# Performance work log

Measured on AMD Instinct MI355X. Metric: run time of the kernel, lower is better.

The kernel has to match this reference:

```python
import jax, jax.numpy as jnp
import numpy as np

BETA = 0.9
THRESH = 1.0
SLOPE = 25.0  # fast_sigmoid surrogate slope

@jax.custom_vjp
def spike(x):
    # forward: heaviside(mem - threshold); backward: fast-sigmoid surrogate
    return (x > 0).astype(x.dtype)

def _spike_fwd(x):
    return (x > 0).astype(x.dtype), x

def _spike_bwd(x, g):
    return (g / (SLOPE * jnp.abs(x) + 1.0) ** 2,)

spike.defvjp(_spike_fwd, _spike_bwd)

def lif_step(mem, cur):
    # snntorch Leaky, reset_mechanism='subtract': reset from previous mem (detached)
    reset = jax.lax.stop_gradient((mem > THRESH).astype(cur.dtype))
    mem_new = BETA * mem + cur - reset * THRESH
    spk = spike(mem_new - THRESH)
    return spk, mem_new

def setup_inputs() -> dict:
    key = jax.random.key(0)
    ks = jax.random.split(key, 10)
    B, S, T = 256, 8, 25
    A, V, H, E = 512, 512, 256, 128
    a_seq = (jax.random.uniform(ks[0], (B, S, T, A)) < 0.2).astype(jnp.float32)
    v_seq = (jax.random.uniform(ks[1], (B, S, T, V)) < 0.2).astype(jnp.float32)
    def lin(kw, kb, out_d, in_d):
        lim = 1.0 / np.sqrt(in_d)
        W = jax.random.uniform(kw, (out_d, in_d), minval=-lim, maxval=lim, dtype=jnp.float32)
        b = jax.random.uniform(kb, (out_d,), minval=-lim, maxval=lim, dtype=jnp.float32)
        return W, b
    W_a1, b_a1 = lin(ks[2], ks[3], H, A)
    W_a2, b_a2 = lin(ks[4], ks[5], E, H)
    W_v1, b_v1 = lin(ks[6], ks[7], H, V)
    W_v2, b_v2 = lin(ks[8], ks[9], E, H)
    return dict(a_seq=a_seq, v_seq=v_seq, W_a1=W_a1, b_a1=b_a1, W_a2=W_a2, b_a2=b_a2,
                W_v1=W_v1, b_v1=b_v1, W_v2=W_v2, b_v2=b_v2)

def reference(a_seq, v_seq, W_a1, b_a1, W_a2, b_a2, W_v1, b_v1, W_v2, b_v2):
    B, S, T, A = a_seq.shape
    V = v_seq.shape[-1]
    H = W_a1.shape[0]
    E = W_a2.shape[0]
    BS = B * S  # segments are independent -> fold into batch
    a = a_seq.reshape(BS, T, A).transpose(1, 0, 2)  # [T, BS, A]
    v = v_seq.reshape(BS, T, V).transpose(1, 0, 2)  # [T, BS, V]

    def step(carry, xs):
        ma1, ma2, mv1, mv2, _, _ = carry
        at, vt = xs
        spk_a1, ma1 = lif_step(ma1, at @ W_a1.T + b_a1)
        spk_a2, ma2 = lif_step(ma2, spk_a1 @ W_a2.T + b_a2)
        spk_v1, mv1 = lif_step(mv1, vt @ W_v1.T + b_v1)
        spk_v2, mv2 = lif_step(mv2, spk_v1 @ W_v2.T + b_v2)
        return (ma1, ma2, mv1, mv2, spk_a2, spk_v2), None

    z = jnp.zeros
    init = (z((BS, H)), z((BS, E)), z((BS, H)), z((BS, E)), z((BS, E)), z((BS, E)))
    (ma1, ma2, mv1, mv2, spk_a2, spk_v2), _ = jax.lax.scan(step, init, (a, v))
    combined = jnp.concatenate([spk_a2, spk_v2], axis=1)  # [BS, 2E]
    norm = jnp.linalg.norm(combined, axis=1, keepdims=True)
    combined = combined / jnp.maximum(norm, 1e-12)  # F.normalize p=2 dim=1
    embs = combined.reshape(B, S, 2 * E)
    return embs.mean(axis=1)  # [B, 2E]
```

## Files before the change

### kernel.cpp

```cpp
#include <hip/hip_runtime.h>


typedef short bf16x8 __attribute__((ext_vector_type(8)));
typedef float f32x4 __attribute__((ext_vector_type(4)));

#define RBIG 51200

__global__ void prep_w(const float* __restrict__ Wa1, const float* __restrict__ Wv1,
                       const float* __restrict__ Wa2, const float* __restrict__ Wv2,
                       unsigned short* __restrict__ W1s, unsigned short* __restrict__ W2s) {
    int idx = blockIdx.x * 256 + threadIdx.x;
    float w;
    unsigned short* dst;
    int K, k;
    if (idx < 262144) {
        int p = idx >> 17, rem = idx & 131071;
        int n = rem >> 9; k = rem & 511; K = 512;
        const float* src = p ? Wv1 : Wa1;
        w = src[(size_t)n * 512 + k];
        dst = W1s + (size_t)p * 256 * 1536 + (size_t)n * 1536;
    } else {
        int j = idx - 262144;
        int p = j >> 15, rem = j & 32767;
        int n = rem >> 8; k = rem & 255; K = 256;
        const float* src = p ? Wv2 : Wa2;
        w = src[(size_t)n * 256 + k];
        dst = W2s + (size_t)p * 128 * 768 + (size_t)n * 768;
    }
    unsigned int u  = __float_as_uint(w);
    unsigned int hi = u & 0xFFFF0000u;
    float r1 = w - __uint_as_float(hi);
    unsigned int mi = __float_as_uint(r1) & 0xFFFF0000u;
    float r2 = r1 - __uint_as_float(mi);
    dst[k]         = (unsigned short)(hi >> 16);
    dst[K + k]     = (unsigned short)(mi >> 16);
    dst[2 * K + k] = (unsigned short)(__float_as_uint(r2) >> 16);
}

template <int KSRC, int NT, bool AF32>
__global__ __launch_bounds__(256, 2) void gemm_spl(
    const void* __restrict__ A0, const void* __restrict__ A1,
    const unsigned short* __restrict__ Ws, float* __restrict__ C) {
    constexpr int KE  = 3 * KSRC;
    constexpr int NKB = KSRC / 64;
    constexpr int NC  = 3 * NKB;

    __shared__ unsigned short As[2][128 * 64];
    __shared__ unsigned short Bs[2][128 * 64];

    const int tid  = threadIdx.x;
    const int bx   = blockIdx.x, by = blockIdx.y, bz = blockIdx.z;
    const int lane = tid & 63, wave = tid >> 6;
    const int wm   = wave >> 1, wn = wave & 1;
    const size_t row0 = (size_t)bx * 128;
    const unsigned short* Wp = Ws + (size_t)bz * NT * KE + (size_t)by * 128 * KE;

    f32x4 acc[4][4];
    f32x4 zz = {0.f, 0.f, 0.f, 0.f};
#pragma unroll
    for (int i = 0; i < 4; ++i)
#pragma unroll
        for (int j = 0; j < 4; ++j) acc[i][j] = zz;

    auto stageA = [&](int buf, int kb) {
        if constexpr (AF32) {
            const float* Ag = (const float*)(bz ? A1 : A0);
#pragma unroll
            for (int j = 0; j < 8; ++j) {
                int lin = tid + (j << 8);
                int row = lin >> 4, f4 = lin & 15;
                float4 v = *(const float4*)(Ag + (row0 + row) * KSRC + kb * 64 + (f4 << 2));
                uint2 pk;
                pk.x = (__float_as_uint(v.y) & 0xFFFF0000u) | (__float_as_uint(v.x) >> 16);
                pk.y = (__float_as_uint(v.w) & 0xFFFF0000u) | (__float_as_uint(v.z) >> 16);
                *(uint2*)&As[buf][row * 64 + (f4 << 2)] = pk;
            }
        } else {
            const unsigned short* Ag = (const unsigned short*)(bz ? A1 : A0);
#pragma unroll
            for (int j = 0; j < 4; ++j) {
                int slot = (tid << 3) + (j << 11);
                int row = slot >> 6, col = slot & 63;
                uint4 v = *(const uint4*)(Ag + (row0 + row) * KSRC + kb * 64 + col);
                *(uint4*)&As[buf][slot] = v;
            }
        }
    };
    auto stageB = [&](int buf, int kb, int s) {
        const unsigned short* Bg = Wp + (size_t)s * KSRC + kb * 64;
#pragma unroll
        for (int j = 0; j < 4; ++j) {
            int slot = (tid << 3) + (j << 11);
            int row = slot >> 6, col = slot & 63;
            uint4 v = *(const uint4*)(Bg + (size_t)row * KE + col);
            *(uint4*)&Bs[buf][slot] = v;
        }
    };

    stageA(0, 0);
    stageB(0, 0, 0);
    int kb = 0, s = 0;
    for (int c = 0; c < NC; ++c) {
        __syncthreads();
        int s1 = s + 1, kb1 = kb;
        if (s1 == 3) { s1 = 0; kb1 = kb + 1; }
        if (c + 1 < NC) {
            stageB((c + 1) & 1, kb1, s1);
            if (s1 == 0) stageA(kb1 & 1, kb1);
        }
        const unsigned short* Ab = As[kb & 1];
        const unsigned short* Bb = Bs[c & 1];
#pragma unroll
        for (int ks = 0; ks < 2; ++ks) {
            int ko = ks * 32 + ((lane >> 4) << 3);
            bf16x8 af[4], bb[4];
#pragma unroll
            for (int mi2 = 0; mi2 < 4; ++mi2)
                af[mi2] = *(const bf16x8*)&Ab[(wm * 64 + mi2 * 16 + (lane & 15)) * 64 + ko];
#pragma unroll
            for (int ni = 0; ni < 4; ++ni)
                bb[ni] = *(const bf16x8*)&Bb[(wn * 64 + ni * 16 + (lane & 15)) * 64 + ko];
#pragma unroll
            for (int mi2 = 0; mi2 < 4; ++mi2)
#pragma unroll
                for (int ni = 0; ni < 4; ++ni)
                    acc[mi2][ni] = __builtin_amdgcn_mfma_f32_16x16x32_bf16(
                        af[mi2], bb[ni], acc[mi2][ni], 0, 0, 0);
        }
        kb = kb1; s = s1;
    }

    float* Cp = C + (size_t)bz * RBIG * NT;
    int r4 = ((lane >> 4) << 2), cl = lane & 15;
#pragma unroll
    for (int mi2 = 0; mi2 < 4; ++mi2)
#pragma unroll
        for (int ni = 0; ni < 4; ++ni) {
            size_t col = (size_t)by * 128 + wn * 64 + ni * 16 + cl;
#pragma unroll
            for (int j = 0; j < 4; ++j) {
                size_t row = row0 + wm * 64 + mi2 * 16 + r4 + j;
                Cp[row * NT + col] = acc[mi2][ni][j];
            }
        }
}

__global__ void lif1_k(const float* __restrict__ cur, const float* __restrict__ ba1,
                       const float* __restrict__ bv1, unsigned int* __restrict__ spk) {
    int r = blockIdx.x, p = blockIdx.y, d = threadIdx.x;
    const float* c0 = cur + ((size_t)p * RBIG + (size_t)r * 25) * 256 + 2 * d;
    const float* bias = p ? bv1 : ba1;
    float b0 = bias[2 * d], b1 = bias[2 * d + 1];
    float2 cv[25];
#pragma unroll
    for (int t = 0; t < 25; ++t) cv[t] = *(const float2*)(c0 + (size_t)t * 256);
    unsigned int* sp = spk + ((size_t)p * RBIG + (size_t)r * 25) * 128 + d;
    float m0 = 0.f, m1 = 0.f;
#pragma unroll
    for (int t = 0; t < 25; ++t) {
        float r0 = (m0 > 1.f) ? 1.f : 0.f;
        float r1 = (m1 > 1.f) ? 1.f : 0.f;
        m0 = 0.9f * m0 + (cv[t].x + b0) - r0;
        m1 = 0.9f * m1 + (cv[t].y + b1) - r1;
        unsigned int w = (m0 > 1.f ? 0x3F80u : 0u) | (m1 > 1.f ? 0x3F800000u : 0u);
        sp[(size_t)t * 128] = w;
    }
}

__global__ void lif2_k(const float* __restrict__ cur2, const float* __restrict__ ba2,
                       const float* __restrict__ bv2, float* __restrict__ spk2) {
    int r = blockIdx.x, p = blockIdx.y, d = threadIdx.x;
    const float* c0 = cur2 + ((size_t)p * RBIG + (size_t)r * 25) * 128 + 2 * d;
    const float* bias = p ? bv2 : ba2;
    float b0 = bias[2 * d], b1 = bias[2 * d + 1];
    float2 cv[25];
#pragma unroll
    for (int t = 0; t < 25; ++t) cv[t] = *(const float2*)(c0 + (size_t)t * 128);
    float m0 = 0.f, m1 = 0.f;
#pragma unroll
    for (int t = 0; t < 25; ++t) {
        float r0 = (m0 > 1.f) ? 1.f : 0.f;
        float r1 = (m1 > 1.f) ? 1.f : 0.f;
        m0 = 0.9f * m0 + (cv[t].x + b0) - r0;
        m1 = 0.9f * m1 + (cv[t].y + b1) - r1;
    }
    float2 o;
    o.x = (m0 > 1.f) ? 1.f : 0.f;
    o.y = (m1 > 1.f) ? 1.f : 0.f;
    *(float2*)(spk2 + ((size_t)p * 2048 + r) * 128 + 2 * d) = o;
}

__global__ void epi_k(const float* __restrict__ spk2, float* __restrict__ out) {
    int b = blockIdx.x, d = threadIdx.x;
    int p = d >> 7, e = d & 127;
    __shared__ float red[256];
    float acc = 0.f;
    for (int s = 0; s < 8; ++s) {
        float v = spk2[((size_t)p * 2048 + (size_t)(b * 8 + s)) * 128 + e];
        red[d] = v * v;
        __syncthreads();
        for (int off = 128; off > 0; off >>= 1) {
            if (d < off) red[d] += red[d + off];
            __syncthreads();
        }
        float nrm = sqrtf(red[0]);
        acc += v / fmaxf(nrm, 1e-12f);
        __syncthreads();
    }
    out[(size_t)b * 256 + d] = acc * 0.125f;
}

extern "C" void kernel_launch(void* const* d_in, const int* in_sizes, int n_in,
                              void* d_out, int out_size, void* d_ws, size_t ws_size,
                              hipStream_t stream) {
    const float* a_seq = (const float*)d_in[0];
    const float* v_seq = (const float*)d_in[1];
    const float* W_a1  = (const float*)d_in[2];
    const float* b_a1  = (const float*)d_in[3];
    const float* W_a2  = (const float*)d_in[4];
    const float* b_a2  = (const float*)d_in[5];
    const float* W_v1  = (const float*)d_in[6];
    const float* b_v1  = (const float*)d_in[7];
    const float* W_v2  = (const float*)d_in[8];
    const float* b_v2  = (const float*)d_in[9];

    char* ws = (char*)d_ws;
    unsigned short* W1s  = (unsigned short*)(ws);
    unsigned short* W2s  = (unsigned short*)(ws + 1572864);
    unsigned short* spk1 = (unsigned short*)(ws + 1966080);
    float*          curb = (float*)(ws + 54394880);
    float*          spk2 = (float*)(ws + 159252480);
    float*          out  = (float*)d_out;

    prep_w<<<1280, 256, 0, stream>>>(W_a1, W_v1, W_a2, W_v2, W1s, W2s);

    gemm_spl<512, 256, true><<<dim3(400, 2, 2), 256, 0, stream>>>(a_seq, v_seq, W1s, curb);
    lif1_k<<<dim3(2048, 2), 128, 0, stream>>>(curb, b_a1, b_v1, (unsigned int*)spk1);

    gemm_spl<256, 128, false><<<dim3(400, 1, 2), 256, 0, stream>>>(
        spk1, spk1 + (size_t)RBIG * 256, W2s, curb);
    lif2_k<<<dim3(2048, 2), 64, 0, stream>>>(curb, b_a2, b_v2, spk2);

    epi_k<<<256, 256, 0, stream>>>(spk2, out);
}
```

Before: 405.3 us.

## Swizzle GEMM LDS tiles and use wave shuffles in epilogue norm

The GEMM's A and B tiles in LDS are now stored with an XOR swizzle on the row index (row&7)<<3, and the MFMA fragment reads apply the matching XOR. This targets bank conflicts when 16 lanes read the same column offset from consecutive 64-element rows. The epilogue L2-norm reduction changes from a shared-memory tree with many barriers to wave shuffles plus a 4-entry partial array. It sums v instead of v*v, which is only equivalent because spikes are 0/1.

```diff
diff --git a/kernel.cpp b/kernel.cpp
--- a/kernel.cpp
+++ b/kernel.cpp
@@ -73,7 +73,8 @@
                 uint2 pk;
                 pk.x = (__float_as_uint(v.y) & 0xFFFF0000u) | (__float_as_uint(v.x) >> 16);
                 pk.y = (__float_as_uint(v.w) & 0xFFFF0000u) | (__float_as_uint(v.z) >> 16);
-                *(uint2*)&As[buf][row * 64 + (f4 << 2)] = pk;
+                int idx = (row * 64 + (f4 << 2)) ^ ((row & 7) << 3);
+                *(uint2*)&As[buf][idx] = pk;
             }
         } else {
             const unsigned short* Ag = (const unsigned short*)(bz ? A1 : A0);
@@ -82,7 +83,8 @@
                 int slot = (tid << 3) + (j << 11);
                 int row = slot >> 6, col = slot & 63;
                 uint4 v = *(const uint4*)(Ag + (row0 + row) * KSRC + kb * 64 + col);
-                *(uint4*)&As[buf][slot] = v;
+                int idx = slot ^ ((row & 7) << 3);
+                *(uint4*)&As[buf][idx] = v;
             }
         }
     };
@@ -93,13 +95,15 @@
             int slot = (tid << 3) + (j << 11);
             int row = slot >> 6, col = slot & 63;
             uint4 v = *(const uint4*)(Bg + (size_t)row * KE + col);
-            *(uint4*)&Bs[buf][slot] = v;
+            int idx = slot ^ ((row & 7) << 3);
+            *(uint4*)&Bs[buf][idx] = v;
         }
     };
 
     stageA(0, 0);
     stageB(0, 0, 0);
     int kb = 0, s = 0;
+    const int swz = (lane & 7) << 3;
     for (int c = 0; c < NC; ++c) {
         __syncthreads();
         int s1 = s + 1, kb1 = kb;
@@ -115,11 +119,15 @@
             int ko = ks * 32 + ((lane >> 4) << 3);
             bf16x8 af[4], bb[4];
 #pragma unroll
-            for (int mi2 = 0; mi2 < 4; ++mi2)
-                af[mi2] = *(const bf16x8*)&Ab[(wm * 64 + mi2 * 16 + (lane & 15)) * 64 + ko];
-#pragma unroll
-            for (int ni = 0; ni < 4; ++ni)
-                bb[ni] = *(const bf16x8*)&Bb[(wn * 64 + ni * 16 + (lane & 15)) * 64 + ko];
+            for (int mi2 = 0; mi2 < 4; ++mi2) {
+                int Rm = wm * 64 + mi2 * 16 + (lane & 15);
+                af[mi2] = *(const bf16x8*)&Ab[(Rm * 64 + ko) ^ swz];
+            }
+#pragma unroll
+            for (int ni = 0; ni < 4; ++ni) {
+                int Rn = wn * 64 + ni * 16 + (lane & 15);
+                bb[ni] = *(const bf16x8*)&Bb[(Rn * 64 + ko) ^ swz];
+            }
 #pragma unroll
             for (int mi2 = 0; mi2 < 4; ++mi2)
 #pragma unroll
@@ -193,17 +201,16 @@
 __global__ void epi_k(const float* __restrict__ spk2, float* __restrict__ out) {
     int b = blockIdx.x, d = threadIdx.x;
     int p = d >> 7, e = d & 127;
-    __shared__ float red[256];
+    __shared__ float part[4];
     float acc = 0.f;
     for (int s = 0; s < 8; ++s) {
         float v = spk2[((size_t)p * 2048 + (size_t)(b * 8 + s)) * 128 + e];
-        red[d] = v * v;
+        float sq = v;
+#pragma unroll
+        for (int off = 32; off > 0; off >>= 1) sq += __shfl_down(sq, off);
+        if ((d & 63) == 0) part[d >> 6] = sq;
         __syncthreads();
-        for (int off = 128; off > 0; off >>= 1) {
-            if (d < off) red[d] += red[d + off];
-            __syncthreads();
-        }
-        float nrm = sqrtf(red[0]);
+        float nrm = sqrtf(part[0] + part[1] + part[2] + part[3]);
         acc += v / fmaxf(nrm, 1e-12f);
         __syncthreads();
     }
```

New measurement: 377.2 us. -6.9%, faster.
